# Performance work log

Hardware: AMD Instinct MI355X
Metric: run time of the kernel (lower is better)

The kernel has to match this reference:

```python
import jax, jax.numpy as jnp
import numpy as np

DIM = 256
NUM_HEADS = 8


def setup_inputs() -> dict:
    key = jax.random.key(0)
    ks = jax.random.split(key, 5)
    B, V, C, H, W = 4, 6, DIM, 64, 64
    x = jax.random.normal(ks[0], (B, V, C, H, W), dtype=jnp.float32)
    # 1x1 conv weights (out_channels, in_channels), bias=False
    s = 1.0 / np.sqrt(C)
    Wq = jax.random.normal(ks[1], (C, C), dtype=jnp.float32) * s
    Wk = jax.random.normal(ks[2], (C, C), dtype=jnp.float32) * s
    Wv = jax.random.normal(ks[3], (C, C), dtype=jnp.float32) * s
    Wo = jax.random.normal(ks[4], (C, C), dtype=jnp.float32) * s
    return {"x": x, "Wq": Wq, "Wk": Wk, "Wv": Wv, "Wo": Wo}


def reference(x, Wq, Wk, Wv, Wo):
    B, V, C, H, W = x.shape
    h = NUM_HEADS
    dh = C // h
    scale = dh ** (-0.5)

    def proj(Wm):
        # 1x1 conv == per-pixel channel matmul; -> [B, h, V, HW, dh]
        t = jnp.einsum('bvchw,oc->bvohw', x, Wm)
        t = t.reshape(B, V, h, dh, H * W)
        return t.transpose(0, 2, 1, 4, 3)  # b h v w d (w = flattened HW)

    Q = proj(Wq)
    K = proj(Wk)
    Vv = proj(Wv)

    Qloc = Q.mean(axis=2)  # average query over views: [B, h, HW, dh]
    scores = jnp.einsum('bhwd,bhvwd->bhwv', Qloc, K) * scale  # [B, h, HW, V]
    attn = jax.nn.softmax(scores, axis=-1)
    out = jnp.einsum('bhwv,bhvwd->bhwd', attn, Vv)  # [B, h, HW, dh]
    out = out.transpose(0, 1, 3, 2).reshape(B, C, H, W)
    return jnp.einsum('bchw,oc->bohw', out, Wo)  # out_proj 1x1 conv
```

## Files before the change

### kernel.cpp

```cpp
#include <hip/hip_runtime.h>
#include <hip/hip_bf16.h>


typedef __bf16 bf16x8 __attribute__((ext_vector_type(8)));
typedef __bf16 bf16x4 __attribute__((ext_vector_type(4)));
typedef float f32x4 __attribute__((ext_vector_type(4)));

#define HW 4096
#define C_DIM 256
#define NV 6
#define NB 4

__global__ __launch_bounds__(256) void convert_weights_kernel(
    const float* __restrict__ Wq, const float* __restrict__ Wk,
    const float* __restrict__ Wv, const float* __restrict__ Wo,
    __hip_bfloat16* __restrict__ out)
{
    const float* srcs[4] = {Wq, Wk, Wv, Wo};
    const int m = blockIdx.y;
    const int i = blockIdx.x * 256 + threadIdx.x;
    out[m * 65536 + i] = __float2bfloat16(srcs[m][i]);
}

__global__ __launch_bounds__(256) void transpose_mean_kernel(
    const float* __restrict__ x,
    __hip_bfloat16* __restrict__ xt,
    __hip_bfloat16* __restrict__ xbar)
{
    __shared__ float tile[64][65];
    const int w0 = blockIdx.x * 64;
    const int c0 = blockIdx.y * 64;
    const int b  = blockIdx.z;
    const int t  = threadIdx.x;
    const int li = t & 63;
    const int qi = t >> 6;
    float acc[16];
#pragma unroll
    for (int i = 0; i < 16; ++i) acc[i] = 0.f;

    for (int v = 0; v < NV; ++v) {
        const float* src = x + (((size_t)b * NV + v) * C_DIM + c0) * HW + w0;
#pragma unroll
        for (int i = 0; i < 16; ++i) {
            const int c = qi + 4 * i;
            tile[li][c] = src[(size_t)c * HW + li];
        }
        __syncthreads();
        __hip_bfloat16* dst = xt + (((size_t)b * NV + v) * HW + w0) * C_DIM + c0;
#pragma unroll
        for (int i = 0; i < 16; ++i) {
            const int w = qi + 4 * i;
            const float val = tile[w][li];
            acc[i] += val;
            dst[(size_t)w * C_DIM + li] = __float2bfloat16(val);
        }
        __syncthreads();
    }
    __hip_bfloat16* dbar = xbar + ((size_t)b * HW + w0) * C_DIM + c0;
#pragma unroll
    for (int i = 0; i < 16; ++i) {
        const int w = qi + 4 * i;
        dbar[(size_t)w * C_DIM + li] = __float2bfloat16(acc[i] * (1.f / 6.f));
    }
}

__global__ __launch_bounds__(512) void mega_kernel(
    const __hip_bfloat16* __restrict__ xt,
    const __hip_bfloat16* __restrict__ xbar,
    const __hip_bfloat16* __restrict__ Wq,
    const __hip_bfloat16* __restrict__ Wk,
    const __hip_bfloat16* __restrict__ Wv,
    const __hip_bfloat16* __restrict__ Wo,
    float* __restrict__ out)
{
    __shared__ __align__(16) __hip_bfloat16 Abuf[2][8320];
    const size_t SL = (size_t)HW * C_DIM;
    const int w0 = blockIdx.x * 32;
    const int b  = blockIdx.y;
    const int t  = threadIdx.x, wv = t >> 6, l = t & 63;
    const int g = l >> 4, rl = l & 15;

    auto stageA = [&](int buf, const __hip_bfloat16* src) {
#pragma unroll
        for (int c2 = 0; c2 < 2; ++c2) {
            const int ch = wv * 2 + c2;
            const int kb = ch * 2 + (l >> 5);
            const __hip_bfloat16* gp = src + (size_t)(w0 + (l & 31)) * 256 + kb * 8;
            __builtin_amdgcn_global_load_lds(
                (const __attribute__((address_space(1))) void*)gp,
                (__attribute__((address_space(3))) void*)(&Abuf[buf][ch * 520]),
                16, 0, 0);
        }
    };

    auto ldA = [&](int buf, int kt, int i) -> bf16x8 {
        const int kb = kt * 4 + g;
        return *(const bf16x8*)&Abuf[buf][(kb >> 1) * 520 + (kb & 1) * 256 + (i * 16 + rl) * 8];
    };
    auto ldB = [&](const __hip_bfloat16* W, int j, int kt) -> bf16x8 {
        return *(const bf16x8*)(W + (size_t)(wv * 32 + j * 16 + rl) * 256 + kt * 32 + g * 8);
    };

    f32x4 Kacc[2][2], Vacc[2][2], oacc[2][2];

    auto gemm1 = [&](int buf, const __hip_bfloat16* W) {
#pragma unroll
        for (int i = 0; i < 2; ++i)
#pragma unroll
            for (int j = 0; j < 2; ++j) {
                Kacc[i][j][0] = 0.f; Kacc[i][j][1] = 0.f;
                Kacc[i][j][2] = 0.f; Kacc[i][j][3] = 0.f;
            }
#pragma unroll
        for (int kt = 0; kt < 8; ++kt) {
            bf16x8 b0 = ldB(W, 0, kt), b1 = ldB(W, 1, kt);
            bf16x8 a0 = ldA(buf, kt, 0), a1 = ldA(buf, kt, 1);
            Kacc[0][0] = __builtin_amdgcn_mfma_f32_16x16x32_bf16(a0, b0, Kacc[0][0], 0, 0, 0);
            Kacc[0][1] = __builtin_amdgcn_mfma_f32_16x16x32_bf16(a0, b1, Kacc[0][1], 0, 0, 0);
            Kacc[1][0] = __builtin_amdgcn_mfma_f32_16x16x32_bf16(a1, b0, Kacc[1][0], 0, 0, 0);
            Kacc[1][1] = __builtin_amdgcn_mfma_f32_16x16x32_bf16(a1, b1, Kacc[1][1], 0, 0, 0);
        }
    };

    auto gemmKV = [&](int buf) {
#pragma unroll
        for (int i = 0; i < 2; ++i)
#pragma unroll
            for (int j = 0; j < 2; ++j) {
#pragma unroll
                for (int r = 0; r < 4; ++r) { Kacc[i][j][r] = 0.f; Vacc[i][j][r] = 0.f; }
            }
#pragma unroll
        for (int kt = 0; kt < 8; ++kt) {
            bf16x8 bk0 = ldB(Wk, 0, kt), bk1 = ldB(Wk, 1, kt);
            bf16x8 bv0 = ldB(Wv, 0, kt), bv1 = ldB(Wv, 1, kt);
            bf16x8 a0 = ldA(buf, kt, 0), a1 = ldA(buf, kt, 1);
            Kacc[0][0] = __builtin_amdgcn_mfma_f32_16x16x32_bf16(a0, bk0, Kacc[0][0], 0, 0, 0);
            Vacc[0][0] = __builtin_amdgcn_mfma_f32_16x16x32_bf16(a0, bv0, Vacc[0][0], 0, 0, 0);
            Kacc[0][1] = __builtin_amdgcn_mfma_f32_16x16x32_bf16(a0, bk1, Kacc[0][1], 0, 0, 0);
            Vacc[0][1] = __builtin_amdgcn_mfma_f32_16x16x32_bf16(a0, bv1, Vacc[0][1], 0, 0, 0);
            Kacc[1][0] = __builtin_amdgcn_mfma_f32_16x16x32_bf16(a1, bk0, Kacc[1][0], 0, 0, 0);
            Vacc[1][0] = __builtin_amdgcn_mfma_f32_16x16x32_bf16(a1, bv0, Vacc[1][0], 0, 0, 0);
            Kacc[1][1] = __builtin_amdgcn_mfma_f32_16x16x32_bf16(a1, bk1, Kacc[1][1], 0, 0, 0);
            Vacc[1][1] = __builtin_amdgcn_mfma_f32_16x16x32_bf16(a1, bv1, Vacc[1][1], 0, 0, 0);
        }
    };

    stageA(0, xbar + (size_t)b * SL);
    __syncthreads();
    gemm1(0, Wq);
    stageA(1, xt + (size_t)(b * NV) * SL);

    const float scale = 0.17677669529663687f;
    bf16x4 qb[2][2];
#pragma unroll
    for (int i = 0; i < 2; ++i)
#pragma unroll
        for (int j = 0; j < 2; ++j)
#pragma unroll
            for (int r = 0; r < 4; ++r)
                qb[i][j][r] = (__bf16)(Kacc[i][j][r] * scale);

    float m[2][4], den[2][4];
#pragma unroll
    for (int i = 0; i < 2; ++i)
#pragma unroll
        for (int r = 0; r < 4; ++r) { m[i][r] = -1e30f; den[i][r] = 0.f; }
#pragma unroll
    for (int i = 0; i < 2; ++i)
#pragma unroll
        for (int j = 0; j < 2; ++j) {
            oacc[i][j][0] = 0.f; oacc[i][j][1] = 0.f;
            oacc[i][j][2] = 0.f; oacc[i][j][3] = 0.f;
        }
    __syncthreads();

    for (int v = 0; v < NV; ++v) {
        const int buf = (v + 1) & 1;
        if (v < NV - 1) stageA(buf ^ 1, xt + (size_t)(b * NV + v + 1) * SL);
        gemmKV(buf);

#pragma unroll
        for (int i = 0; i < 2; ++i)
#pragma unroll
            for (int r = 0; r < 4; ++r) {
                float s = (float)qb[i][0][r] * Kacc[i][0][r]
                        + (float)qb[i][1][r] * Kacc[i][1][r];
                s += __shfl_xor(s, 1);
                s += __shfl_xor(s, 2);
                s += __shfl_xor(s, 4);
                s += __shfl_xor(s, 8);
                const float mn = fmaxf(m[i][r], s);
                const float f  = __expf(m[i][r] - mn);
                const float e  = __expf(s - mn);
                den[i][r] = den[i][r] * f + e;
                m[i][r]   = mn;
#pragma unroll
                for (int j = 0; j < 2; ++j) {
                    oacc[i][j][r] = oacc[i][j][r] * f + e * Vacc[i][j][r];
                }
            }
        __syncthreads();
    }

#pragma unroll
    for (int i = 0; i < 2; ++i)
#pragma unroll
        for (int r = 0; r < 4; ++r) {
            const float inv = 1.f / den[i][r];
            const int row = i * 16 + g * 4 + r;
#pragma unroll
            for (int j = 0; j < 2; ++j) {
                const int c  = wv * 32 + j * 16 + rl;
                const int kb = c >> 3;
                Abuf[0][(kb >> 1) * 520 + (kb & 1) * 256 + row * 8 + (c & 7)] =
                    __float2bfloat16(oacc[i][j][r] * inv);
            }
        }
    __syncthreads();
    gemm1(0, Wo);

    float* op = out + (size_t)b * C_DIM * HW;
#pragma unroll
    for (int i = 0; i < 2; ++i)
#pragma unroll
        for (int j = 0; j < 2; ++j) {
            const int col = wv * 32 + j * 16 + rl;
            *(f32x4*)(op + (size_t)col * HW + w0 + i * 16 + g * 4) = Kacc[i][j];
        }
}

extern "C" void kernel_launch(void* const* d_in, const int* in_sizes, int n_in,
                              void* d_out, int out_size, void* d_ws, size_t ws_size,
                              hipStream_t stream)
{
    const float* x  = (const float*)d_in[0];
    const float* Wq = (const float*)d_in[1];
    const float* Wk = (const float*)d_in[2];
    const float* Wv = (const float*)d_in[3];
    const float* Wo = (const float*)d_in[4];
    (void)in_sizes; (void)n_in; (void)out_size; (void)ws_size;

    char* ws = (char*)d_ws;
    const size_t MB = 1024ull * 1024ull;
    const size_t SL = (size_t)HW * C_DIM;

    __hip_bfloat16* Wbf  = (__hip_bfloat16*)(ws);
    __hip_bfloat16* xt   = (__hip_bfloat16*)(ws + 1 * MB);
    __hip_bfloat16* xbar = (__hip_bfloat16*)(ws + 49 * MB);

    const __hip_bfloat16* WqB = Wbf;
    const __hip_bfloat16* WkB = Wbf + 65536;
    const __hip_bfloat16* WvB = Wbf + 131072;
    const __hip_bfloat16* WoB = Wbf + 196608;

    convert_weights_kernel<<<dim3(256, 4), 256, 0, stream>>>(Wq, Wk, Wv, Wo, Wbf);
    transpose_mean_kernel<<<dim3(HW / 64, C_DIM / 64, NB), 256, 0, stream>>>(x, xt, xbar);
    mega_kernel<<<dim3(HW / 32, NB), 512, 0, stream>>>(xt, xbar, WqB, WkB, WvB, WoB, (float*)d_out);
}
```

Before: 107.7 us.

## Split K and V projections across separate wave groups in 1024-thread blocks

```diff
diff --git a/kernel.cpp b/kernel.cpp
--- a/kernel.cpp
+++ b/kernel.cpp
@@ -64,7 +64,7 @@
     }
 }
 
-__global__ __launch_bounds__(512) void mega_kernel(
+__global__ __launch_bounds__(1024, 4) void mega_kernel(
     const __hip_bfloat16* __restrict__ xt,
     const __hip_bfloat16* __restrict__ xbar,
     const __hip_bfloat16* __restrict__ Wq,
@@ -73,7 +73,9 @@
     const __hip_bfloat16* __restrict__ Wo,
     float* __restrict__ out)
 {
-    __shared__ __align__(16) __hip_bfloat16 Abuf[2][8320];
+    __shared__ __align__(16) __hip_bfloat16 Abuf[2][8192];
+    __shared__ float ef_lds[2][8][32][2];
+    __shared__ float inv_lds[8][32];
     const size_t SL = (size_t)HW * C_DIM;
     const int w0 = blockIdx.x * 32;
     const int b  = blockIdx.y;
@@ -81,29 +83,30 @@
     const int g = l >> 4, rl = l & 15;
 
     auto stageA = [&](int buf, const __hip_bfloat16* src) {
-#pragma unroll
-        for (int c2 = 0; c2 < 2; ++c2) {
-            const int ch = wv * 2 + c2;
-            const int kb = ch * 2 + (l >> 5);
-            const __hip_bfloat16* gp = src + (size_t)(w0 + (l & 31)) * 256 + kb * 8;
-            __builtin_amdgcn_global_load_lds(
-                (const __attribute__((address_space(1))) void*)gp,
-                (__attribute__((address_space(3))) void*)(&Abuf[buf][ch * 520]),
-                16, 0, 0);
-        }
+        const __hip_bfloat16* gp =
+            src + (size_t)(w0 + (l & 31)) * 256 + (wv * 2 + (l >> 5)) * 8;
+        __builtin_amdgcn_global_load_lds(
+            (const __attribute__((address_space(1))) void*)gp,
+            (__attribute__((address_space(3))) void*)(&Abuf[buf][wv * 512]),
+            16, 0, 0);
     };
-
     auto ldA = [&](int buf, int kt, int i) -> bf16x8 {
-        const int kb = kt * 4 + g;
-        return *(const bf16x8*)&Abuf[buf][(kb >> 1) * 520 + (kb & 1) * 256 + (i * 16 + rl) * 8];
+        return *(const bf16x8*)&Abuf[buf][(kt * 4 + g) * 256 + (i * 16 + rl) * 8];
     };
-    auto ldB = [&](const __hip_bfloat16* W, int j, int kt) -> bf16x8 {
-        return *(const bf16x8*)(W + (size_t)(wv * 32 + j * 16 + rl) * 256 + kt * 32 + g * 8);
-    };
-
-    f32x4 Kacc[2][2], Vacc[2][2], oacc[2][2];
-
-    auto gemm1 = [&](int buf, const __hip_bfloat16* W) {
+
+    if (wv < 8) {
+        const int h = wv;
+        bf16x8 bkreg[8][2];
+#pragma unroll
+        for (int kt = 0; kt < 8; ++kt)
+#pragma unroll
+            for (int j = 0; j < 2; ++j)
+                bkreg[kt][j] = *(const bf16x8*)(Wk + (size_t)(h * 32 + j * 16 + rl) * 256 + kt * 32 + g * 8);
+        stageA(0, xt + (size_t)(b * NV) * SL);
+        stageA(1, xbar + (size_t)b * SL);
+        __syncthreads();
+
+        f32x4 Kacc[2][2];
 #pragma unroll
         for (int i = 0; i < 2; ++i)
 #pragma unroll
@@ -113,121 +116,166 @@
             }
 #pragma unroll
         for (int kt = 0; kt < 8; ++kt) {
-            bf16x8 b0 = ldB(W, 0, kt), b1 = ldB(W, 1, kt);
-            bf16x8 a0 = ldA(buf, kt, 0), a1 = ldA(buf, kt, 1);
+            bf16x8 b0 = *(const bf16x8*)(Wq + (size_t)(h * 32 + rl) * 256 + kt * 32 + g * 8);
+            bf16x8 b1 = *(const bf16x8*)(Wq + (size_t)(h * 32 + 16 + rl) * 256 + kt * 32 + g * 8);
+            bf16x8 a0 = ldA(1, kt, 0), a1 = ldA(1, kt, 1);
             Kacc[0][0] = __builtin_amdgcn_mfma_f32_16x16x32_bf16(a0, b0, Kacc[0][0], 0, 0, 0);
             Kacc[0][1] = __builtin_amdgcn_mfma_f32_16x16x32_bf16(a0, b1, Kacc[0][1], 0, 0, 0);
             Kacc[1][0] = __builtin_amdgcn_mfma_f32_16x16x32_bf16(a1, b0, Kacc[1][0], 0, 0, 0);
             Kacc[1][1] = __builtin_amdgcn_mfma_f32_16x16x32_bf16(a1, b1, Kacc[1][1], 0, 0, 0);
         }
-    };
-
-    auto gemmKV = [&](int buf) {
+        const float scale = 0.17677669529663687f;
+        bf16x4 qb[2][2];
+#pragma unroll
+        for (int i = 0; i < 2; ++i)
+#pragma unroll
+            for (int j = 0; j < 2; ++j)
+#pragma unroll
+                for (int r = 0; r < 4; ++r)
+                    qb[i][j][r] = (__bf16)(Kacc[i][j][r] * scale);
+        float m[2][4], den[2][4];
+#pragma unroll
+        for (int i = 0; i < 2; ++i)
+#pragma unroll
+            for (int r = 0; r < 4; ++r) { m[i][r] = -1e30f; den[i][r] = 0.f; }
+        __syncthreads();
+
+        for (int v = 0; v < NV; ++v) {
+            const int buf = v & 1;
+            if (v < NV - 1) stageA(buf ^ 1, xt + (size_t)(b * NV + v + 1) * SL);
+#pragma unroll
+            for (int i = 0; i < 2; ++i)
+#pragma unroll
+                for (int j = 0; j < 2; ++j) {
+                    Kacc[i][j][0] = 0.f; Kacc[i][j][1] = 0.f;
+                    Kacc[i][j][2] = 0.f; Kacc[i][j][3] = 0.f;
+                }
+#pragma unroll
+            for (int kt = 0; kt < 8; ++kt) {
+                bf16x8 a0 = ldA(buf, kt, 0), a1 = ldA(buf, kt, 1);
+                Kacc[0][0] = __builtin_amdgcn_mfma_f32_16x16x32_bf16(a0, bkreg[kt][0], Kacc[0][0], 0, 0, 0);
+                Kacc[0][1] = __builtin_amdgcn_mfma_f32_16x16x32_bf16(a0, bkreg[kt][1], Kacc[0][1], 0, 0, 0);
+                Kacc[1][0] = __builtin_amdgcn_mfma_f32_16x16x32_bf16(a1, bkreg[kt][0], Kacc[1][0], 0, 0, 0);
+                Kacc[1][1] = __builtin_amdgcn_mfma_f32_16x16x32_bf16(a1, bkreg[kt][1], Kacc[1][1], 0, 0, 0);
+            }
+#pragma unroll
+            for (int i = 0; i < 2; ++i)
+#pragma unroll
+                for (int r = 0; r < 4; ++r) {
+                    float s = (float)qb[i][0][r] * Kacc[i][0][r]
+                            + (float)qb[i][1][r] * Kacc[i][1][r];
+                    s += __shfl_xor(s, 1);
+                    s += __shfl_xor(s, 2);
+                    s += __shfl_xor(s, 4);
+                    s += __shfl_xor(s, 8);
+                    const float mn = fmaxf(m[i][r], s);
+                    const float f  = __expf(m[i][r] - mn);
+                    const float e  = __expf(s - mn);
+                    den[i][r] = den[i][r] * f + e;
+                    m[i][r]   = mn;
+                    if (rl == 0) {
+                        const int row = i * 16 + g * 4 + r;
+                        ef_lds[buf][h][row][0] = e;
+                        ef_lds[buf][h][row][1] = f;
+                    }
+                }
+            __syncthreads();
+        }
+#pragma unroll
+        for (int i = 0; i < 2; ++i)
+#pragma unroll
+            for (int r = 0; r < 4; ++r)
+                if (rl == 0) inv_lds[h][i * 16 + g * 4 + r] = 1.f / den[i][r];
+        __syncthreads();
+        __syncthreads();
+    } else {
+        const int h = wv - 8;
+        bf16x8 bvreg[8][2];
+#pragma unroll
+        for (int kt = 0; kt < 8; ++kt)
+#pragma unroll
+            for (int j = 0; j < 2; ++j)
+                bvreg[kt][j] = *(const bf16x8*)(Wv + (size_t)(h * 32 + j * 16 + rl) * 256 + kt * 32 + g * 8);
+        stageA(0, xt + (size_t)(b * NV) * SL);
+        stageA(1, xbar + (size_t)b * SL);
+        __syncthreads();
+
+        f32x4 oacc[2][2];
 #pragma unroll
         for (int i = 0; i < 2; ++i)
 #pragma unroll
             for (int j = 0; j < 2; ++j) {
-#pragma unroll
-                for (int r = 0; r < 4; ++r) { Kacc[i][j][r] = 0.f; Vacc[i][j][r] = 0.f; }
-            }
-#pragma unroll
-        for (int kt = 0; kt < 8; ++kt) {
-            bf16x8 bk0 = ldB(Wk, 0, kt), bk1 = ldB(Wk, 1, kt);
-            bf16x8 bv0 = ldB(Wv, 0, kt), bv1 = ldB(Wv, 1, kt);
-            bf16x8 a0 = ldA(buf, kt, 0), a1 = ldA(buf, kt, 1);
-            Kacc[0][0] = __builtin_amdgcn_mfma_f32_16x16x32_bf16(a0, bk0, Kacc[0][0], 0, 0, 0);
-            Vacc[0][0] = __builtin_amdgcn_mfma_f32_16x16x32_bf16(a0, bv0, Vacc[0][0], 0, 0, 0);
-            Kacc[0][1] = __builtin_amdgcn_mfma_f32_16x16x32_bf16(a0, bk1, Kacc[0][1], 0, 0, 0);
-            Vacc[0][1] = __builtin_amdgcn_mfma_f32_16x16x32_bf16(a0, bv1, Vacc[0][1], 0, 0, 0);
-            Kacc[1][0] = __builtin_amdgcn_mfma_f32_16x16x32_bf16(a1, bk0, Kacc[1][0], 0, 0, 0);
-            Vacc[1][0] = __builtin_amdgcn_mfma_f32_16x16x32_bf16(a1, bv0, Vacc[1][0], 0, 0, 0);
-            Kacc[1][1] = __builtin_amdgcn_mfma_f32_16x16x32_bf16(a1, bk1, Kacc[1][1], 0, 0, 0);
-            Vacc[1][1] = __builtin_amdgcn_mfma_f32_16x16x32_bf16(a1, bv1, Vacc[1][1], 0, 0, 0);
-        }
-    };
-
-    stageA(0, xbar + (size_t)b * SL);
-    __syncthreads();
-    gemm1(0, Wq);
-    stageA(1, xt + (size_t)(b * NV) * SL);
-
-    const float scale = 0.17677669529663687f;
-    bf16x4 qb[2][2];
+                oacc[i][j][0] = 0.f; oacc[i][j][1] = 0.f;
+                oacc[i][j][2] = 0.f; oacc[i][j][3] = 0.f;
+            }
+        __syncthreads();
+
+        for (int v = 0; v < NV; ++v) {
+            const int buf = v & 1;
+            if (v < NV - 1) stageA(buf ^ 1, xt + (size_t)(b * NV + v + 1) * SL);
+            f32x4 Vacc[2][2];
+#pragma unroll
+            for (int i = 0; i < 2; ++i)
+#pragma unroll
+                for (int j = 0; j < 2; ++j) {
+                    Vacc[i][j][0] = 0.f; Vacc[i][j][1] = 0.f;
+                    Vacc[i][j][2] = 0.f; Vacc[i][j][3] = 0.f;
+                }
+#pragma unroll
+            for (int kt = 0; kt < 8; ++kt) {
+                bf16x8 a0 = ldA(buf, kt, 0), a1 = ldA(buf, kt, 1);
+                Vacc[0][0] = __builtin_amdgcn_mfma_f32_16x16x32_bf16(a0, bvreg[kt][0], Vacc[0][0], 0, 0, 0);
+                Vacc[0][1] = __builtin_amdgcn_mfma_f32_16x16x32_bf16(a0, bvreg[kt][1], Vacc[0][1], 0, 0, 0);
+                Vacc[1][0] = __builtin_amdgcn_mfma_f32_16x16x32_bf16(a1, bvreg[kt][0], Vacc[1][0], 0, 0, 0);
+                Vacc[1][1] = __builtin_amdgcn_mfma_f32_16x16x32_bf16(a1, bvreg[kt][1], Vacc[1][1], 0, 0, 0);
+            }
+            __syncthreads();
+#pragma unroll
+            for (int i = 0; i < 2; ++i)
+#pragma unroll
+                for (int r = 0; r < 4; ++r) {
+                    const int row = i * 16 + g * 4 + r;
+                    const float e = ef_lds[buf][h][row][0];
+                    const float f = ef_lds[buf][h][row][1];
+#pragma unroll
+                    for (int j = 0; j < 2; ++j)
+                        oacc[i][j][r] = oacc[i][j][r] * f + e * Vacc[i][j][r];
+                }
+        }
+        __syncthreads();
+#pragma unroll
+        for (int i = 0; i < 2; ++i)
+#pragma unroll
+            for (int r = 0; r < 4; ++r) {
+                const int row = i * 16 + g * 4 + r;
+                const float inv = inv_lds[h][row];
+#pragma unroll
+                for (int j = 0; j < 2; ++j) {
+                    const int c = h * 32 + j * 16 + rl;
+                    Abuf[0][(c >> 3) * 256 + row * 8 + (c & 7)] =
+                        __float2bfloat16(oacc[i][j][r] * inv);
+                }
+            }
+        __syncthreads();
+    }
+
+    f32x4 acc2[2];
+#pragma unroll
+    for (int i = 0; i < 2; ++i) {
+        acc2[i][0] = 0.f; acc2[i][1] = 0.f; acc2[i][2] = 0.f; acc2[i][3] = 0.f;
+    }
+#pragma unroll
+    for (int kt = 0; kt < 8; ++kt) {
+        bf16x8 bo = *(const bf16x8*)(Wo + (size_t)(wv * 16 + rl) * 256 + kt * 32 + g * 8);
+        bf16x8 a0 = ldA(0, kt, 0), a1 = ldA(0, kt, 1);
+        acc2[0] = __builtin_amdgcn_mfma_f32_16x16x32_bf16(a0, bo, acc2[0], 0, 0, 0);
+        acc2[1] = __builtin_amdgcn_mfma_f32_16x16x32_bf16(a1, bo, acc2[1], 0, 0, 0);
+    }
+    float* op = out + (size_t)b * C_DIM * HW;
+    const int col = wv * 16 + rl;
 #pragma unroll
     for (int i = 0; i < 2; ++i)
-#pragma unroll
-        for (int j = 0; j < 2; ++j)
-#pragma unroll
-            for (int r = 0; r < 4; ++r)
-                qb[i][j][r] = (__bf16)(Kacc[i][j][r] * scale);
-
-    float m[2][4], den[2][4];
-#pragma unroll
-    for (int i = 0; i < 2; ++i)
-#pragma unroll
-        for (int r = 0; r < 4; ++r) { m[i][r] = -1e30f; den[i][r] = 0.f; }
-#pragma unroll
-    for (int i = 0; i < 2; ++i)
-#pragma unroll
-        for (int j = 0; j < 2; ++j) {
-            oacc[i][j][0] = 0.f; oacc[i][j][1] = 0.f;
-            oacc[i][j][2] = 0.f; oacc[i][j][3] = 0.f;
-        }
-    __syncthreads();
-
-    for (int v = 0; v < NV; ++v) {
-        const int buf = (v + 1) & 1;
-        if (v < NV - 1) stageA(buf ^ 1, xt + (size_t)(b * NV + v + 1) * SL);
-        gemmKV(buf);
-
-#pragma unroll
-        for (int i = 0; i < 2; ++i)
-#pragma unroll
-            for (int r = 0; r < 4; ++r) {
-                float s = (float)qb[i][0][r] * Kacc[i][0][r]
-                        + (float)qb[i][1][r] * Kacc[i][1][r];
-                s += __shfl_xor(s, 1);
-                s += __shfl_xor(s, 2);
-                s += __shfl_xor(s, 4);
-                s += __shfl_xor(s, 8);
-                const float mn = fmaxf(m[i][r], s);
-                const float f  = __expf(m[i][r] - mn);
-                const float e  = __expf(s - mn);
-                den[i][r] = den[i][r] * f + e;
-                m[i][r]   = mn;
-#pragma unroll
-                for (int j = 0; j < 2; ++j) {
-                    oacc[i][j][r] = oacc[i][j][r] * f + e * Vacc[i][j][r];
-                }
-            }
-        __syncthreads();
-    }
-
-#pragma unroll
-    for (int i = 0; i < 2; ++i)
-#pragma unroll
-        for (int r = 0; r < 4; ++r) {
-            const float inv = 1.f / den[i][r];
-            const int row = i * 16 + g * 4 + r;
-#pragma unroll
-            for (int j = 0; j < 2; ++j) {
-                const int c  = wv * 32 + j * 16 + rl;
-                const int kb = c >> 3;
-                Abuf[0][(kb >> 1) * 520 + (kb & 1) * 256 + row * 8 + (c & 7)] =
-                    __float2bfloat16(oacc[i][j][r] * inv);
-            }
-        }
-    __syncthreads();
-    gemm1(0, Wo);
-
-    float* op = out + (size_t)b * C_DIM * HW;
-#pragma unroll
-    for (int i = 0; i < 2; ++i)
-#pragma unroll
-        for (int j = 0; j < 2; ++j) {
-            const int col = wv * 32 + j * 16 + rl;
-            *(f32x4*)(op + (size_t)col * HW + w0 + i * 16 + g * 4) = Kacc[i][j];
-        }
+        *(f32x4*)(op + (size_t)col * HW + w0 + i * 16 + g * 4) = acc2[i];
 }
 
 extern "C" void kernel_launch(void* const* d_in, const int* in_sizes, int n_in,
@@ -256,5 +304,5 @@
 
     convert_weights_kernel<<<dim3(256, 4), 256, 0, stream>>>(Wq, Wk, Wv, Wo, Wbf);
     transpose_mean_kernel<<<dim3(HW / 64, C_DIM / 64, NB), 256, 0, stream>>>(x, xt, xbar);
-    mega_kernel<<<dim3(HW / 32, NB), 512, 0, stream>>>(xt, xbar, WqB, WkB, WvB, WoB, (float*)d_out);
+    mega_kernel<<<dim3(HW / 32, NB), 1024, 0, stream>>>(xt, xbar, WqB, WkB, WvB, WoB, (float*)d_out);
 }
```

New measurement: 139.4 us, median of 2. 29.4% more time.
